# Optimization experiments

Hardware: AMD Instinct MI355X
Metric: run time of the kernel (lower is better)

The kernel has to match this reference:

```python
import jax, jax.numpy as jnp
import numpy as np

T, N, E, IN, ED, H, B, HEADS, L, DFF, OUT = 16, 6400, 65536, 128, 16, 256, 64, 8, 2, 2048, 8
DH = H // HEADS


def _layernorm(x, g, b, eps=1e-5):
    m = jnp.mean(x, -1, keepdims=True)
    v = jnp.var(x, -1, keepdims=True)
    return (x - m) * jax.lax.rsqrt(v + eps) * g + b


def setup_inputs() -> dict:
    key = jax.random.key(0)
    ks = iter(jax.random.split(key, 48))

    def w(shape):
        fan_in = shape[-2] if len(shape) >= 2 else shape[-1]
        return jax.random.normal(next(ks), shape, jnp.float32) * (fan_in ** -0.5)

    inp = {
        "x": jax.random.normal(next(ks), (T, N, IN), jnp.float32),
        "edge_attr": jax.random.normal(next(ks), (T, E, ED), jnp.float32),
        "edge_index": jax.random.randint(next(ks), (T, 2, E), 0, N),
        "batch": jnp.sort(jax.random.randint(next(ks), (T, N), 0, B), axis=-1),
        # EdgeSAGEConv layer 0: msg_in = IN + ED
        "neigh_w0": w((IN + ED, H)), "neigh_b0": jnp.zeros((H,)),
        "root_w0": w((IN, H)), "root_b0": jnp.zeros((H,)),
        "ln_g0": jnp.ones((H,)), "ln_b0": jnp.zeros((H,)),
        # EdgeSAGEConv layer 1: msg_in = H + ED
        "neigh_w1": w((H + ED, H)), "neigh_b1": jnp.zeros((H,)),
        "root_w1": w((H, H)), "root_b1": jnp.zeros((H,)),
        "ln_g1": jnp.ones((H,)), "ln_b1": jnp.zeros((H,)),
        # NodeAttentionPool
        "pool_proj_w": w((H, H)), "pool_proj_b": jnp.zeros((H,)),
        "pool_score_w": w((H, 1)), "pool_score_b": jnp.zeros((1,)),
        # temporal transformer
        "pos_emb": jax.random.normal(next(ks), (T + 1, H), jnp.float32) * 0.02,
        "cls_token": jax.random.normal(next(ks), (1, 1, H), jnp.float32) * 0.02,
        "tx_qkv_w": w((L, H, 3 * H)), "tx_qkv_b": jnp.zeros((L, 3 * H)),
        "tx_out_w": w((L, H, H)), "tx_out_b": jnp.zeros((L, H)),
        "tx_ff1_w": w((L, H, DFF)), "tx_ff1_b": jnp.zeros((L, DFF)),
        "tx_ff2_w": w((L, DFF, H)), "tx_ff2_b": jnp.zeros((L, H)),
        "tx_ln1_g": jnp.ones((L, H)), "tx_ln1_b": jnp.zeros((L, H)),
        "tx_ln2_g": jnp.ones((L, H)), "tx_ln2_b": jnp.zeros((L, H)),
        "head_w": w((H, OUT)), "head_b": jnp.zeros((OUT,)),
    }
    return inp


def reference(x, edge_attr, edge_index, batch,
              neigh_w0, neigh_b0, root_w0, root_b0, ln_g0, ln_b0,
              neigh_w1, neigh_b1, root_w1, root_b1, ln_g1, ln_b1,
              pool_proj_w, pool_proj_b, pool_score_w, pool_score_b,
              pos_emb, cls_token,
              tx_qkv_w, tx_qkv_b, tx_out_w, tx_out_b,
              tx_ff1_w, tx_ff1_b, tx_ff2_w, tx_ff2_b,
              tx_ln1_g, tx_ln1_b, tx_ln2_g, tx_ln2_b,
              head_w, head_b):
    def conv(h, src, dst, ea, wn, bn, wr, br):
        # message: gather x_j, concat edge_attr, linear; aggregate mean at dst
        msg = jnp.concatenate([h[src], ea], -1) @ wn + bn            # [E, H]
        agg = jax.ops.segment_sum(msg, dst, num_segments=N)
        cnt = jax.ops.segment_sum(jnp.ones((dst.shape[0], 1), h.dtype), dst, num_segments=N)
        return agg / jnp.maximum(cnt, 1.0) + h @ wr + br

    def day(xd, eid, ead, bd):
        src, dst = eid[0], eid[1]
        h = _layernorm(jax.nn.relu(conv(xd, src, dst, ead, neigh_w0, neigh_b0, root_w0, root_b0)), ln_g0, ln_b0)
        h = _layernorm(jax.nn.relu(conv(h, src, dst, ead, neigh_w1, neigh_b1, root_w1, root_b1)), ln_g1, ln_b1)
        # segment softmax attention pooling over graphs
        s = (jnp.tanh(h @ pool_proj_w + pool_proj_b) @ pool_score_w + pool_score_b)[:, 0]
        smax = jax.ops.segment_max(s, bd, num_segments=B)
        e = jnp.exp(s - smax[bd])
        wgt = e / jax.ops.segment_sum(e, bd, num_segments=B)[bd]
        return jax.ops.segment_sum(h * wgt[:, None], bd, num_segments=B)  # [B, H]

    Hd = jax.vmap(day)(x, edge_index, edge_attr, batch)               # [T, B, H]
    seq = jnp.transpose(Hd, (1, 0, 2))                                # [B, T, H]
    cls = jnp.broadcast_to(cls_token, (seq.shape[0], 1, H))
    seq = jnp.concatenate([cls, seq], 1) + pos_emb[None]              # [B, T+1, H]
    Bb, S = seq.shape[0], seq.shape[1]
    for l in range(L):  # post-norm TransformerEncoderLayer, relu FFN
        qkv = seq @ tx_qkv_w[l] + tx_qkv_b[l]
        q, k, v = [t.reshape(Bb, S, HEADS, DH) for t in jnp.split(qkv, 3, -1)]
        att = jax.nn.softmax(jnp.einsum('bqhd,bkhd->bhqk', q, k) / (DH ** 0.5), axis=-1)
        o = jnp.einsum('bhqk,bkhd->bqhd', att, v).reshape(Bb, S, H) @ tx_out_w[l] + tx_out_b[l]
        seq = _layernorm(seq + o, tx_ln1_g[l], tx_ln1_b[l])
        f = jax.nn.relu(seq @ tx_ff1_w[l] + tx_ff1_b[l]) @ tx_ff2_w[l] + tx_ff2_b[l]
        seq = _layernorm(seq + f, tx_ln2_g[l], tx_ln2_b[l])
    return jax.nn.softplus(seq[:, 0] @ head_w + head_b)               # [B, OUT]
```

## Files before the change

### kernel.cpp

```cpp
#include <hip/hip_runtime.h>
#include <math.h>

#define T_ 16
#define N_ 6400
#define E_ 65536
#define IN_ 128
#define ED_ 16
#define H_ 256
#define B_ 64
#define HEADS_ 8
#define L_ 2
#define DFF_ 2048
#define OUT_ 8
#define DH_ 32
#define S_ 17
#define M_TX (B_ * S_)

typedef unsigned short u16;
typedef short bf16x8 __attribute__((ext_vector_type(8)));
typedef float f32x4 __attribute__((ext_vector_type(4)));

__device__ __forceinline__ u16 f2bf(float x) {
  unsigned u = __float_as_uint(x);
  unsigned r = (u + 0x7FFFu + ((u >> 16) & 1)) >> 16;
  return (u16)r;
}
__device__ __forceinline__ float bf2f(u16 h) {
  return __uint_as_float(((unsigned)h) << 16);
}

__global__ void zero_k(float* __restrict__ p, long n) {
  long i = (long)blockIdx.x * 256 + threadIdx.x;
  if (i < n) p[i] = 0.f;
}

__global__ void split_k(const float* __restrict__ in, u16* __restrict__ h,
                        u16* __restrict__ l, long n) {
  long i = (long)blockIdx.x * 256 + threadIdx.x;
  if (i < n) {
    const float v = in[i];
    const u16 hi = f2bf(v);
    h[i] = hi;
    l[i] = f2bf(v - bf2f(hi));
  }
}

__launch_bounds__(256) __global__
void wconv_k(const float* __restrict__ W, int K, int Nc, u16* __restrict__ Th,
             u16* __restrict__ Tl, int row_off, int ldk) {
  __shared__ float s[16][17];
  const int kt = blockIdx.y * 16, nt = blockIdx.x * 16;
  const int a = threadIdx.x >> 4, b2 = threadIdx.x & 15;
  s[a][b2] = W[(long)(kt + a) * Nc + nt + b2];
  __syncthreads();
  const float v = s[b2][a];
  const u16 hi = f2bf(v);
  const long o = (long)(row_off + nt + a) * ldk + kt + b2;
  Th[o] = hi;
  Tl[o] = f2bf(v - bf2f(hi));
}

__global__ void biascat_k(const float* __restrict__ b1, const float* __restrict__ b2,
                          float* __restrict__ o) {
  const int i = threadIdx.x;
  o[i] = (i < 256) ? b1[i] : b2[i - 256];
}

template <int EP, int SPLITK, int OUTBF>
__launch_bounds__(256) __global__
void gemm_bf(const u16* __restrict__ Ahb, const u16* __restrict__ Alb, long az,
             const u16* __restrict__ Wth, const u16* __restrict__ Wtl,
             const float* __restrict__ bias,
             float* __restrict__ Ob, u16* __restrict__ Ohb, u16* __restrict__ Olb,
             long oz, int K, int Nc, int ldo) {
  const u16 *Ah, *Al;
  float* O = nullptr;
  u16 *Oh = nullptr, *Ol = nullptr;
  int kbeg, kend;
  if (SPLITK == 1) {
    Ah = Ahb + (long)blockIdx.z * az;
    Al = Alb + (long)blockIdx.z * az;
    if (Ob) O = Ob + (long)blockIdx.z * oz;
    if (Ohb) {
      Oh = Ohb + (long)blockIdx.z * oz;
      Ol = Olb + (long)blockIdx.z * oz;
    }
    kbeg = 0;
    kend = K;
  } else {
    Ah = Ahb;
    Al = Alb;
    O = Ob;
    const int ch = K / SPLITK;
    kbeg = blockIdx.z * ch;
    kend = kbeg + ch;
  }
  const int n0 = blockIdx.x * 128;
  const int m0 = blockIdx.y * 64;
  const int tid = threadIdx.x;
  const int lane = tid & 63;
  const int wave = tid >> 6;
  const int wm = wave & 1;
  const int wn = wave >> 1;
  const int r15 = lane & 15;
  const int q8 = (lane >> 4) << 3;
  const int quad4 = (lane >> 4) << 2;

  __shared__ u16 As_h[64 * 40], As_l[64 * 40];
  __shared__ u16 Bs_h[128 * 40], Bs_l[128 * 40];

  f32x4 acc[2][4];
#pragma unroll
  for (int i = 0; i < 2; ++i)
#pragma unroll
    for (int j = 0; j < 4; ++j) acc[i][j] = (f32x4){0.f, 0.f, 0.f, 0.f};

  const int a_row = tid >> 2;
  const int a_kq = (tid & 3) << 3;
  const int b_row = tid >> 1;
  const int b_kq = (tid & 1) << 4;

  for (int k0 = kbeg; k0 < kend; k0 += 32) {
    const bf16x8 avh = *(const bf16x8*)(Ah + (long)(m0 + a_row) * K + k0 + a_kq);
    const bf16x8 avl = *(const bf16x8*)(Al + (long)(m0 + a_row) * K + k0 + a_kq);
    const long wb = (long)(n0 + b_row) * K + k0 + b_kq;
    const bf16x8 bvh0 = *(const bf16x8*)(Wth + wb);
    const bf16x8 bvh1 = *(const bf16x8*)(Wth + wb + 8);
    const bf16x8 bvl0 = *(const bf16x8*)(Wtl + wb);
    const bf16x8 bvl1 = *(const bf16x8*)(Wtl + wb + 8);
    __syncthreads();
    *(bf16x8*)&As_h[a_row * 40 + a_kq] = avh;
    *(bf16x8*)&As_l[a_row * 40 + a_kq] = avl;
    *(bf16x8*)&Bs_h[b_row * 40 + b_kq] = bvh0;
    *(bf16x8*)&Bs_h[b_row * 40 + b_kq + 8] = bvh1;
    *(bf16x8*)&Bs_l[b_row * 40 + b_kq] = bvl0;
    *(bf16x8*)&Bs_l[b_row * 40 + b_kq + 8] = bvl1;
    __syncthreads();
    bf16x8 ah[2], al[2], bh[4], bl[4];
#pragma unroll
    for (int i = 0; i < 2; ++i) {
      const int ao = (wm * 32 + i * 16 + r15) * 40 + q8;
      ah[i] = *(const bf16x8*)&As_h[ao];
      al[i] = *(const bf16x8*)&As_l[ao];
    }
#pragma unroll
    for (int j = 0; j < 4; ++j) {
      const int bo = (wn * 64 + j * 16 + r15) * 40 + q8;
      bh[j] = *(const bf16x8*)&Bs_h[bo];
      bl[j] = *(const bf16x8*)&Bs_l[bo];
    }
#pragma unroll
    for (int i = 0; i < 2; ++i)
#pragma unroll
      for (int j = 0; j < 4; ++j) {
        acc[i][j] = __builtin_amdgcn_mfma_f32_16x16x32_bf16(ah[i], bh[j], acc[i][j], 0, 0, 0);
        acc[i][j] = __builtin_amdgcn_mfma_f32_16x16x32_bf16(ah[i], bl[j], acc[i][j], 0, 0, 0);
        acc[i][j] = __builtin_amdgcn_mfma_f32_16x16x32_bf16(al[i], bh[j], acc[i][j], 0, 0, 0);
      }
  }

#pragma unroll
  for (int i = 0; i < 2; ++i) {
#pragma unroll
    for (int j = 0; j < 4; ++j) {
      const int col = n0 + wn * 64 + j * 16 + r15;
      const int rbase = m0 + wm * 32 + i * 16 + quad4;
      const float bv = bias ? bias[col] : 0.f;
#pragma unroll
      for (int r = 0; r < 4; ++r) {
        float v = acc[i][j][r];
        if (SPLITK == 1) {
          v += bv;
          if (EP == 1) v = fmaxf(v, 0.f);
          if (EP == 2) v = tanhf(v);
          if (OUTBF) {
            const u16 hi = f2bf(v);
            Oh[(long)(rbase + r) * ldo + col] = hi;
            Ol[(long)(rbase + r) * ldo + col] = f2bf(v - bf2f(hi));
          } else {
            O[(long)(rbase + r) * ldo + col] = v;
          }
        } else {
          if (blockIdx.z == 0) v += bv;
          atomicAdd(&O[(long)(rbase + r) * ldo + col], v);
        }
      }
    }
  }
}

__launch_bounds__(256) __global__
void gemm_k(const float* __restrict__ Abase, long az,
            const float* __restrict__ W,
            const float* __restrict__ addbase, long adz,
            float* __restrict__ Obase, long oz, int K, int Nc, int ldo) {
  const float* A = Abase + (long)blockIdx.z * az;
  const float* addp = addbase + (long)blockIdx.z * adz;
  float* O = Obase + (long)blockIdx.z * oz;
  const int n0 = blockIdx.x * 64;
  const int m0 = blockIdx.y * 64;
  const int tid = threadIdx.x;
  const int tx = tid & 15, ty = tid >> 4;
  __shared__ float As[16][64];
  __shared__ float Ws[16][64];
  float acc[4][4] = {{0.f, 0.f, 0.f, 0.f}, {0.f, 0.f, 0.f, 0.f},
                     {0.f, 0.f, 0.f, 0.f}, {0.f, 0.f, 0.f, 0.f}};
  const int ar = tid >> 2;
  const int ak = (tid & 3) << 2;
  const int wr = tid >> 4;
  const int wc = (tid & 15) << 2;
  for (int k0 = 0; k0 < K; k0 += 16) {
    const float4 av = *(const float4*)(A + (long)(m0 + ar) * K + k0 + ak);
    const float4 wv = *(const float4*)(W + (long)(k0 + wr) * Nc + n0 + wc);
    __syncthreads();
    As[ak + 0][ar] = av.x;
    As[ak + 1][ar] = av.y;
    As[ak + 2][ar] = av.z;
    As[ak + 3][ar] = av.w;
    *(float4*)(&Ws[wr][wc]) = wv;
    __syncthreads();
#pragma unroll
    for (int kk = 0; kk < 16; ++kk) {
      const float4 a4 = *(const float4*)(&As[kk][ty << 2]);
      const float4 b4 = *(const float4*)(&Ws[kk][tx << 2]);
      const float aa[4] = {a4.x, a4.y, a4.z, a4.w};
      const float bb[4] = {b4.x, b4.y, b4.z, b4.w};
#pragma unroll
      for (int i = 0; i < 4; ++i)
#pragma unroll
        for (int j = 0; j < 4; ++j) acc[i][j] = fmaf(aa[i], bb[j], acc[i][j]);
    }
  }
#pragma unroll
  for (int i = 0; i < 4; ++i) {
    const int m = m0 + (ty << 2) + i;
    float o[4];
#pragma unroll
    for (int j = 0; j < 4; ++j)
      o[j] = acc[i][j] + addp[(long)m * ldo + n0 + (tx << 2) + j];
    *(float4*)(O + (long)m * ldo + n0 + (tx << 2)) = make_float4(o[0], o[1], o[2], o[3]);
  }
}

__global__ void deg_k(const int* __restrict__ eib, int* __restrict__ deg, int t0) {
  const int z = blockIdx.y;
  const int e = blockIdx.x * 256 + threadIdx.x;
  const int dst = eib[(long)(t0 + z) * 2 * E_ + E_ + e];
  atomicAdd(&deg[z * N_ + dst], 1);
}

__launch_bounds__(256) __global__
void scan_k(const int* __restrict__ deg, int* __restrict__ offs, int* __restrict__ cursor) {
  const int z = blockIdx.x, tid = threadIdx.x;
  const int* d = deg + (long)z * N_;
  const int base = tid * 25;
  int loc[25];
  int s = 0;
#pragma unroll
  for (int i = 0; i < 25; ++i) {
    loc[i] = s;
    s += d[base + i];
  }
  __shared__ int ps[256];
  ps[tid] = s;
  __syncthreads();
  for (int off = 1; off < 256; off <<= 1) {
    int v = 0;
    if (tid >= off) v = ps[tid - off];
    __syncthreads();
    if (tid >= off) ps[tid] += v;
    __syncthreads();
  }
  const int pre = (tid == 0) ? 0 : ps[tid - 1];
#pragma unroll
  for (int i = 0; i < 25; ++i) {
    const int o = pre + loc[i];
    offs[(long)z * (N_ + 1) + base + i] = o;
    cursor[(long)z * N_ + base + i] = o;
  }
  if (tid == 255) offs[(long)z * (N_ + 1) + N_] = ps[255];
}

__global__ void fill_k(const int* __restrict__ eib, int* __restrict__ cursor,
                       int* __restrict__ elist, int* __restrict__ srcs, int t0) {
  const int z = blockIdx.y;
  const int e = blockIdx.x * 256 + threadIdx.x;
  const int* base = eib + (long)(t0 + z) * 2 * E_;
  const int src = base[e];
  const int dst = base[E_ + e];
  const int slot = atomicAdd(&cursor[z * N_ + dst], 1);
  elist[(long)z * E_ + slot] = e;
  srcs[(long)z * E_ + slot] = src;
}

__global__ void bounds_k(const int* __restrict__ batchb, int* __restrict__ gb, int t0) {
  const int z = blockIdx.x;
  const int g = threadIdx.x;
  if (g > B_) return;
  const int* bt = batchb + (long)(t0 + z) * N_;
  int lo = 0, hi = N_;
  while (lo < hi) {
    const int mid = (lo + hi) >> 1;
    if (bt[mid] < g) lo = mid + 1; else hi = mid;
  }
  gb[z * (B_ + 1) + g] = lo;
}

__launch_bounds__(256) __global__
void eagg_k(const float* __restrict__ eab, const int* __restrict__ elist,
            const int* __restrict__ offs, float* __restrict__ eaggc, int t0) {
  const int z = blockIdx.y;
  const int ln = threadIdx.x >> 4;
  const int c = threadIdx.x & 15;
  const int n = blockIdx.x * 16 + ln;
  const int beg = offs[(long)z * (N_ + 1) + n];
  const int end = offs[(long)z * (N_ + 1) + n + 1];
  const float* ea = eab + (long)(t0 + z) * E_ * ED_;
  const int* el = elist + (long)z * E_;
  float v = 0.f;
  for (int j = beg; j < end; ++j) v += ea[(long)el[j] * ED_ + c];
  eaggc[((long)z * N_ + n) * ED_ + c] = v / fmaxf((float)(end - beg), 1.f);
}

__launch_bounds__(256) __global__
void conv_gather_k(const float* __restrict__ F, const int* __restrict__ srcs,
                   const int* __restrict__ offs, const float* __restrict__ g,
                   const float* __restrict__ bb, u16* __restrict__ outh,
                   u16* __restrict__ outl) {
  const int z = blockIdx.y;
  const int wid = threadIdx.x >> 6;
  const int lane = threadIdx.x & 63;
  const int n = blockIdx.x * 4 + wid;
  const int beg = offs[(long)z * (N_ + 1) + n];
  const int end = offs[(long)z * (N_ + 1) + n + 1];
  const int* sp = srcs + (long)z * E_;
  const float* Fz = F + (long)z * N_ * 512;
  const int co = lane << 2;
  float4 v = make_float4(0.f, 0.f, 0.f, 0.f);
  int j = beg;
  for (; j + 1 < end; j += 2) {
    const int s0 = sp[j], s1 = sp[j + 1];
    const float4 a = *(const float4*)(Fz + (long)s0 * 512 + co);
    const float4 b2 = *(const float4*)(Fz + (long)s1 * 512 + co);
    v.x += a.x + b2.x;
    v.y += a.y + b2.y;
    v.z += a.z + b2.z;
    v.w += a.w + b2.w;
  }
  if (j < end) {
    const float4 a = *(const float4*)(Fz + (long)sp[j] * 512 + co);
    v.x += a.x;
    v.y += a.y;
    v.z += a.z;
    v.w += a.w;
  }
  const float inv = 1.f / fmaxf((float)(end - beg), 1.f);
  const float4 p = *(const float4*)(Fz + (long)n * 512 + 256 + co);
  const float o0 = fmaxf(fmaf(v.x, inv, p.x), 0.f);
  const float o1 = fmaxf(fmaf(v.y, inv, p.y), 0.f);
  const float o2 = fmaxf(fmaf(v.z, inv, p.z), 0.f);
  const float o3 = fmaxf(fmaf(v.w, inv, p.w), 0.f);
  float s = o0 + o1 + o2 + o3;
  float q = o0 * o0 + o1 * o1 + o2 * o2 + o3 * o3;
#pragma unroll
  for (int m = 1; m < 64; m <<= 1) {
    s += __shfl_xor(s, m, 64);
    q += __shfl_xor(q, m, 64);
  }
  const float mean = s * (1.f / H_);
  const float var = q * (1.f / H_) - mean * mean;
  const float r = rsqrtf(var + 1e-5f);
  const float4 gg = *(const float4*)(g + co);
  const float4 bv = *(const float4*)(bb + co);
  float o[4];
  o[0] = (o0 - mean) * r * gg.x + bv.x;
  o[1] = (o1 - mean) * r * gg.y + bv.y;
  o[2] = (o2 - mean) * r * gg.z + bv.z;
  o[3] = (o3 - mean) * r * gg.w + bv.w;
  const long row = ((long)z * N_ + n) * H_ + co;
  ushort4 hv, lv;
  hv.x = f2bf(o[0]); lv.x = f2bf(o[0] - bf2f(hv.x));
  hv.y = f2bf(o[1]); lv.y = f2bf(o[1] - bf2f(hv.y));
  hv.z = f2bf(o[2]); lv.z = f2bf(o[2] - bf2f(hv.z));
  hv.w = f2bf(o[3]); lv.w = f2bf(o[3] - bf2f(hv.w));
  *(ushort4*)(outh + row) = hv;
  *(ushort4*)(outl + row) = lv;
}

__launch_bounds__(256) __global__
void score_k(const float* __restrict__ tnh, const float* __restrict__ sw,
             const float* __restrict__ sb, float* __restrict__ sbuf) {
  const long z = blockIdx.y;
  const int n = blockIdx.x, c = threadIdx.x;
  float p = tnh[(z * N_ + n) * (long)H_ + c] * sw[c];
  __shared__ float rs[256];
  rs[c] = p;
  __syncthreads();
  for (int s = 128; s > 0; s >>= 1) {
    if (c < s) rs[c] += rs[c + s];
    __syncthreads();
  }
  if (c == 0) sbuf[z * N_ + n] = rs[0] + sb[0];
}

__launch_bounds__(256) __global__
void pool_k(const u16* __restrict__ hh, const u16* __restrict__ hl,
            const float* __restrict__ sbuf, const int* __restrict__ gb,
            float* __restrict__ pooled, int t0) {
  const int z = blockIdx.y;
  const int g = blockIdx.x;
  const int c = threadIdx.x;
  const int beg = gb[z * (B_ + 1) + g];
  const int end = gb[z * (B_ + 1) + g + 1];
  const float* sz = sbuf + (long)z * N_;
  __shared__ float red[256];
  float m = -1e30f;
  for (int i = beg + c; i < end; i += 256) m = fmaxf(m, sz[i]);
  red[c] = m;
  __syncthreads();
  for (int s = 128; s > 0; s >>= 1) {
    if (c < s) red[c] = fmaxf(red[c], red[c + s]);
    __syncthreads();
  }
  m = red[0];
  __syncthreads();
  float sum = 0.f;
  for (int i = beg + c; i < end; i += 256) sum += expf(sz[i] - m);
  red[c] = sum;
  __syncthreads();
  for (int s = 128; s > 0; s >>= 1) {
    if (c < s) red[c] += red[c + s];
    __syncthreads();
  }
  sum = red[0];
  float acc = 0.f;
  for (int i = beg; i < end; ++i) {
    const float w = expf(sz[i] - m);
    const long idx = ((long)z * N_ + i) * H_ + c;
    acc = fmaf(bf2f(hh[idx]) + bf2f(hl[idx]), w, acc);
  }
  pooled[((long)(t0 + z) * B_ + g) * H_ + c] = (sum > 0.f) ? acc / sum : 0.f;
}

__global__ void build_seq_k(const float* __restrict__ pooled, const float* __restrict__ cls,
                            const float* __restrict__ pos, float* __restrict__ seq,
                            u16* __restrict__ sh, u16* __restrict__ sl) {
  const int s = blockIdx.x, b = blockIdx.y, c = threadIdx.x;
  const float v0 = (s == 0) ? cls[c] : pooled[(((long)(s - 1)) * B_ + b) * H_ + c];
  const float v = v0 + pos[(long)s * H_ + c];
  const long o = ((long)b * S_ + s) * H_ + c;
  seq[o] = v;
  const u16 hi = f2bf(v);
  sh[o] = hi;
  sl[o] = f2bf(v - bf2f(hi));
}

__launch_bounds__(256) __global__
void attn_k(const float* __restrict__ qkv, u16* __restrict__ oh, u16* __restrict__ ol) {
  const int b = blockIdx.x, h = blockIdx.y;
  __shared__ float qs[S_][DH_], ks[S_][DH_], vs[S_][DH_], att[S_][S_];
  const int tid = threadIdx.x;
  for (int i = tid; i < S_ * DH_; i += 256) {
    const int s = i / DH_, d = i % DH_;
    const long base = ((long)b * S_ + s) * (3 * H_) + h * DH_ + d;
    qs[s][d] = qkv[base];
    ks[s][d] = qkv[base + H_];
    vs[s][d] = qkv[base + 2 * H_];
  }
  __syncthreads();
  for (int i = tid; i < S_ * S_; i += 256) {
    const int r = i / S_, c2 = i % S_;
    float acc = 0.f;
#pragma unroll
    for (int d = 0; d < DH_; ++d) acc = fmaf(qs[r][d], ks[c2][d], acc);
    att[r][c2] = acc * 0.17677669529663687f;
  }
  __syncthreads();
  if (tid < S_) {
    float m = -1e30f;
    for (int j = 0; j < S_; ++j) m = fmaxf(m, att[tid][j]);
    float sum = 0.f;
    for (int j = 0; j < S_; ++j) {
      const float e = expf(att[tid][j] - m);
      att[tid][j] = e;
      sum += e;
    }
    const float inv = 1.f / sum;
    for (int j = 0; j < S_; ++j) att[tid][j] *= inv;
  }
  __syncthreads();
  for (int i = tid; i < S_ * DH_; i += 256) {
    const int s = i / DH_, d = i % DH_;
    float acc = 0.f;
#pragma unroll
    for (int j = 0; j < S_; ++j) acc = fmaf(att[s][j], vs[j][d], acc);
    const long o = ((long)b * S_ + s) * H_ + h * DH_ + d;
    const u16 hi = f2bf(acc);
    oh[o] = hi;
    ol[o] = f2bf(acc - bf2f(hi));
  }
}

__launch_bounds__(256) __global__
void resid_ln_k(float* __restrict__ seq, const float* __restrict__ add,
                const float* __restrict__ g, const float* __restrict__ bb,
                u16* __restrict__ sh, u16* __restrict__ sl) {
  const int row = blockIdx.x, c = threadIdx.x;
  const float v = seq[(long)row * H_ + c] + add[(long)row * H_ + c];
  __shared__ float rs[256], rq[256];
  rs[c] = v;
  rq[c] = v * v;
  __syncthreads();
  for (int s = 128; s > 0; s >>= 1) {
    if (c < s) {
      rs[c] += rs[c + s];
      rq[c] += rq[c + s];
    }
    __syncthreads();
  }
  const float mean = rs[0] * (1.f / H_);
  const float var = rq[0] * (1.f / H_) - mean * mean;
  const float o = (v - mean) * rsqrtf(var + 1e-5f) * g[c] + bb[c];
  const long idx = (long)row * H_ + c;
  seq[idx] = o;
  const u16 hi = f2bf(o);
  sh[idx] = hi;
  sl[idx] = f2bf(o - bf2f(hi));
}

__launch_bounds__(256) __global__
void head_k(const float* __restrict__ seq, const float* __restrict__ hw,
            const float* __restrict__ hb, float* __restrict__ out) {
  const int b = blockIdx.x, c = threadIdx.x;
  const float x = seq[(long)b * S_ * H_ + c];
  __shared__ float rs[256];
  for (int o = 0; o < OUT_; ++o) {
    rs[c] = x * hw[c * OUT_ + o];
    __syncthreads();
    for (int s = 128; s > 0; s >>= 1) {
      if (c < s) rs[c] += rs[c + s];
      __syncthreads();
    }
    if (c == 0) {
      const float v = rs[0] + hb[o];
      out[b * OUT_ + o] = fmaxf(v, 0.f) + log1pf(expf(-fabsf(v)));
    }
    __syncthreads();
  }
}

extern "C" void kernel_launch(void* const* d_in, const int* in_sizes, int n_in,
                              void* d_out, int out_size, void* d_ws, size_t ws_size,
                              hipStream_t stream) {
  const float* x = (const float*)d_in[0];
  const float* ea = (const float*)d_in[1];
  const int* ei = (const int*)d_in[2];
  const int* batch = (const int*)d_in[3];
  const float* nw0 = (const float*)d_in[4];
  const float* nb0 = (const float*)d_in[5];
  const float* rw0 = (const float*)d_in[6];
  const float* rb0 = (const float*)d_in[7];
  const float* lg0 = (const float*)d_in[8];
  const float* lb0 = (const float*)d_in[9];
  const float* nw1 = (const float*)d_in[10];
  const float* nb1 = (const float*)d_in[11];
  const float* rw1 = (const float*)d_in[12];
  const float* rb1 = (const float*)d_in[13];
  const float* lg1 = (const float*)d_in[14];
  const float* lb1 = (const float*)d_in[15];
  const float* ppw = (const float*)d_in[16];
  const float* ppb = (const float*)d_in[17];
  const float* psw = (const float*)d_in[18];
  const float* psb = (const float*)d_in[19];
  const float* pos = (const float*)d_in[20];
  const float* cls = (const float*)d_in[21];
  const float* qkvw = (const float*)d_in[22];
  const float* qkvbias = (const float*)d_in[23];
  const float* outw = (const float*)d_in[24];
  const float* outb = (const float*)d_in[25];
  const float* f1w = (const float*)d_in[26];
  const float* f1b = (const float*)d_in[27];
  const float* f2w = (const float*)d_in[28];
  const float* f2b = (const float*)d_in[29];
  const float* l1g = (const float*)d_in[30];
  const float* l1b = (const float*)d_in[31];
  const float* l2g = (const float*)d_in[32];
  const float* l2b = (const float*)d_in[33];
  const float* hw = (const float*)d_in[34];
  const float* hb = (const float*)d_in[35];
  float* out = (float*)d_out;

  char* cur = (char*)d_ws;
  auto alloc = [&](long bytes) {
    char* p = cur;
    cur += (bytes + 255) & ~255L;
    return (void*)p;
  };
  float* pooled = (float*)alloc((long)T_ * B_ * H_ * 4);
  float* seq = (float*)alloc((long)M_TX * H_ * 4);
  u16* seqh = (u16*)alloc((long)M_TX * H_ * 2);
  u16* seql = (u16*)alloc((long)M_TX * H_ * 2);
  float* qkvbuf = (float*)alloc((long)M_TX * 3 * H_ * 4);
  float* obuf_f = (float*)alloc((long)M_TX * H_ * 4);
  u16* obufh = (u16*)alloc((long)M_TX * H_ * 2);
  u16* obufl = (u16*)alloc((long)M_TX * H_ * 2);
  u16* ffh = (u16*)alloc((long)M_TX * DFF_ * 2);
  u16* ffl = (u16*)alloc((long)M_TX * DFF_ * 2);
  u16* w0ch = (u16*)alloc(512L * 128 * 2);
  u16* w0cl = (u16*)alloc(512L * 128 * 2);
  u16* w1ch = (u16*)alloc(512L * 256 * 2);
  u16* w1cl = (u16*)alloc(512L * 256 * 2);
  u16* ppwh = (u16*)alloc(256L * 256 * 2);
  u16* ppwl = (u16*)alloc(256L * 256 * 2);
  u16* qkvwh = (u16*)alloc((long)L_ * 768 * 256 * 2);
  u16* qkvwl = (u16*)alloc((long)L_ * 768 * 256 * 2);
  u16* outwh = (u16*)alloc((long)L_ * 256 * 256 * 2);
  u16* outwl = (u16*)alloc((long)L_ * 256 * 256 * 2);
  u16* f1wh = (u16*)alloc((long)L_ * 2048 * 256 * 2);
  u16* f1wl = (u16*)alloc((long)L_ * 2048 * 256 * 2);
  u16* f2wh = (u16*)alloc((long)L_ * 256 * 2048 * 2);
  u16* f2wl = (u16*)alloc((long)L_ * 256 * 2048 * 2);
  float* bias0c = (float*)alloc(512 * 4);
  float* bias1c = (float*)alloc(512 * 4);
  const long fixed_used = cur - (char*)d_ws;

  const long perday = (long)N_ * 128 * 2 * 2
                      + (long)N_ * 512 * 4
                      + (long)N_ * 256 * 2 * 2
                      + (long)N_ * 4
                      + (long)N_ * 16 * 4
                      + (2L * E_ + 3L * N_ + (N_ + 1) + (B_ + 1)) * 4 + 4096;
  int DT = 16;
  while (DT > 1 && (size_t)(fixed_used + (long)DT * perday) > ws_size) DT >>= 1;

  u16* xh = (u16*)alloc((long)DT * N_ * 128 * 2);
  u16* xl = (u16*)alloc((long)DT * N_ * 128 * 2);
  float* bufF = (float*)alloc((long)DT * N_ * 512 * 4);
  u16* bufDh = (u16*)alloc((long)DT * N_ * 256 * 2);
  u16* bufDl = (u16*)alloc((long)DT * N_ * 256 * 2);
  float* sbuf = (float*)alloc((long)DT * N_ * 4);
  float* eaggc = (float*)alloc((long)DT * N_ * 16 * 4);
  int* elist = (int*)alloc((long)DT * E_ * 4);
  int* srcs = (int*)alloc((long)DT * E_ * 4);
  int* offs = (int*)alloc((long)DT * (N_ + 1) * 4);
  int* cursor = (int*)alloc((long)DT * N_ * 4);
  int* deg = (int*)alloc((long)DT * N_ * 4);
  int* gb = (int*)alloc((long)DT * (B_ + 1) * 4);

  auto zero = [&](float* p, long n) {
    zero_k<<<dim3((unsigned)((n + 255) / 256)), 256, 0, stream>>>(p, n);
  };

  wconv_k<<<dim3(16, 8), 256, 0, stream>>>(nw0, 128, 256, w0ch, w0cl, 0, 128);
  wconv_k<<<dim3(16, 8), 256, 0, stream>>>(rw0, 128, 256, w0ch, w0cl, 256, 128);
  wconv_k<<<dim3(16, 16), 256, 0, stream>>>(nw1, 256, 256, w1ch, w1cl, 0, 256);
  wconv_k<<<dim3(16, 16), 256, 0, stream>>>(rw1, 256, 256, w1ch, w1cl, 256, 256);
  wconv_k<<<dim3(16, 16), 256, 0, stream>>>(ppw, 256, 256, ppwh, ppwl, 0, 256);
  for (int l = 0; l < L_; ++l) {
    wconv_k<<<dim3(48, 16), 256, 0, stream>>>(qkvw + (long)l * 256 * 768, 256, 768,
                                              qkvwh + (long)l * 768 * 256,
                                              qkvwl + (long)l * 768 * 256, 0, 256);
    wconv_k<<<dim3(16, 16), 256, 0, stream>>>(outw + (long)l * 256 * 256, 256, 256,
                                              outwh + (long)l * 256 * 256,
                                              outwl + (long)l * 256 * 256, 0, 256);
    wconv_k<<<dim3(128, 16), 256, 0, stream>>>(f1w + (long)l * 256 * 2048, 256, 2048,
                                               f1wh + (long)l * 2048 * 256,
                                               f1wl + (long)l * 2048 * 256, 0, 256);
    wconv_k<<<dim3(16, 128), 256, 0, stream>>>(f2w + (long)l * 2048 * 256, 2048, 256,
                                               f2wh + (long)l * 256 * 2048,
                                               f2wl + (long)l * 256 * 2048, 0, 2048);
  }
  biascat_k<<<1, 512, 0, stream>>>(nb0, rb0, bias0c);
  biascat_k<<<1, 512, 0, stream>>>(nb1, rb1, bias1c);

  for (int t0 = 0; t0 < T_; t0 += DT) {
    const int zc = DT;
    zero((float*)deg, (long)zc * N_);
    deg_k<<<dim3(E_ / 256, zc), 256, 0, stream>>>(ei, deg, t0);
    scan_k<<<dim3(zc), 256, 0, stream>>>(deg, offs, cursor);
    fill_k<<<dim3(E_ / 256, zc), 256, 0, stream>>>(ei, cursor, elist, srcs, t0);
    bounds_k<<<dim3(zc), 128, 0, stream>>>(batch, gb, t0);
    eagg_k<<<dim3(N_ / 16, zc), 256, 0, stream>>>(ea, elist, offs, eaggc, t0);
    {
      const long nx = (long)zc * N_ * 128;
      split_k<<<dim3((unsigned)(nx / 256)), 256, 0, stream>>>(
          x + (long)t0 * N_ * IN_, xh, xl, nx);
    }
    gemm_bf<0, 1, 0><<<dim3(4, N_ / 64, zc), 256, 0, stream>>>(
        xh, xl, (long)N_ * 128, w0ch, w0cl, bias0c, bufF, nullptr, nullptr,
        (long)N_ * 512, 128, 512, 512);
    gemm_k<<<dim3(4, N_ / 64, zc), 256, 0, stream>>>(
        eaggc, (long)N_ * 16, nw0 + (long)IN_ * H_, bufF + 256, (long)N_ * 512,
        bufF + 256, (long)N_ * 512, 16, 256, 512);
    conv_gather_k<<<dim3(N_ / 4, zc), 256, 0, stream>>>(bufF, srcs, offs, lg0, lb0,
                                                        bufDh, bufDl);
    gemm_bf<0, 1, 0><<<dim3(4, N_ / 64, zc), 256, 0, stream>>>(
        bufDh, bufDl, (long)N_ * 256, w1ch, w1cl, bias1c, bufF, nullptr, nullptr,
        (long)N_ * 512, 256, 512, 512);
    gemm_k<<<dim3(4, N_ / 64, zc), 256, 0, stream>>>(
        eaggc, (long)N_ * 16, nw1 + (long)H_ * H_, bufF + 256, (long)N_ * 512,
        bufF + 256, (long)N_ * 512, 16, 256, 512);
    conv_gather_k<<<dim3(N_ / 4, zc), 256, 0, stream>>>(bufF, srcs, offs, lg1, lb1,
                                                        bufDh, bufDl);
    gemm_bf<2, 1, 0><<<dim3(2, N_ / 64, zc), 256, 0, stream>>>(
        bufDh, bufDl, (long)N_ * 256, ppwh, ppwl, ppb, bufF, nullptr, nullptr,
        (long)N_ * 256, 256, 256, 256);
    score_k<<<dim3(N_, zc), 256, 0, stream>>>(bufF, psw, psb, sbuf);
    pool_k<<<dim3(B_, zc), 256, 0, stream>>>(bufDh, bufDl, sbuf, gb, pooled, t0);
  }

  build_seq_k<<<dim3(S_, B_), 256, 0, stream>>>(pooled, cls, pos, seq, seqh, seql);
  for (int l = 0; l < L_; ++l) {
    gemm_bf<0, 1, 0><<<dim3(6, M_TX / 64, 1), 256, 0, stream>>>(
        seqh, seql, 0, qkvwh + (long)l * 768 * 256, qkvwl + (long)l * 768 * 256,
        qkvbias + (long)l * 768, qkvbuf, nullptr, nullptr, 0, 256, 768, 768);
    attn_k<<<dim3(B_, HEADS_), 256, 0, stream>>>(qkvbuf, obufh, obufl);
    gemm_bf<0, 1, 0><<<dim3(2, M_TX / 64, 1), 256, 0, stream>>>(
        obufh, obufl, 0, outwh + (long)l * 256 * 256, outwl + (long)l * 256 * 256,
        outb + (long)l * H_, obuf_f, nullptr, nullptr, 0, 256, 256, 256);
    resid_ln_k<<<dim3(M_TX), 256, 0, stream>>>(seq, obuf_f, l1g + (long)l * H_,
                                               l1b + (long)l * H_, seqh, seql);
    gemm_bf<1, 1, 1><<<dim3(16, M_TX / 64, 1), 256, 0, stream>>>(
        seqh, seql, 0, f1wh + (long)l * 2048 * 256, f1wl + (long)l * 2048 * 256,
        f1b + (long)l * DFF_, nullptr, ffh, ffl, 0, 256, 2048, 2048);
    zero(obuf_f, (long)M_TX * H_);
    gemm_bf<0, 8, 0><<<dim3(2, M_TX / 64, 8), 256, 0, stream>>>(
        ffh, ffl, 0, f2wh + (long)l * 256 * 2048, f2wl + (long)l * 256 * 2048,
        f2b + (long)l * H_, obuf_f, nullptr, nullptr, 0, 2048, 256, 256);
    resid_ln_k<<<dim3(M_TX), 256, 0, stream>>>(seq, obuf_f, l2g + (long)l * H_,
                                               l2b + (long)l * H_, seqh, seql);
  }
  head_k<<<dim3(B_), 256, 0, stream>>>(seq, hw, hb, out);
}
```

Baseline: 1.355 ms.

## Fold edge aggregates into GEMM K-dim, fuse pool score, drop LDS staging

Edge-attribute means are written as extra K columns (padded to 160/288) of the bf16 activation buffers, and the weights gain matching rows. This removes the separate fp32 gemm_k passes that added the edge contribution. The attention-pool score (tanh, dot with the score weight, sum) moves into the projection GEMM epilogue via shuffles and atomics, so the tanh buffer write and score_k go away. The GEMM now loads operands straight from global memory with no shared-memory tiles or barriers. That trades LDS reuse for more global and L2 traffic, and the atomic score adds ordering nondeterminism and drops the score bias, which softmax cancels anyway.

```diff
diff --git a/kernel.cpp b/kernel.cpp
--- a/kernel.cpp
+++ b/kernel.cpp
@@ -33,21 +33,27 @@
   long i = (long)blockIdx.x * 256 + threadIdx.x;
   if (i < n) p[i] = 0.f;
 }
-
-__global__ void split_k(const float* __restrict__ in, u16* __restrict__ h,
-                        u16* __restrict__ l, long n) {
+__global__ void wzero_k(u16* __restrict__ p, long n) {
+  long i = (long)blockIdx.x * 256 + threadIdx.x;
+  if (i < n) p[i] = 0;
+}
+
+__global__ void splitx_k(const float* __restrict__ in, u16* __restrict__ h,
+                         u16* __restrict__ l, long n) {
   long i = (long)blockIdx.x * 256 + threadIdx.x;
   if (i < n) {
+    const long row = i >> 7;
+    const int c = (int)(i & 127);
     const float v = in[i];
     const u16 hi = f2bf(v);
-    h[i] = hi;
-    l[i] = f2bf(v - bf2f(hi));
-  }
-}
-
-__launch_bounds__(256) __global__
-void wconv_k(const float* __restrict__ W, int K, int Nc, u16* __restrict__ Th,
-             u16* __restrict__ Tl, int row_off, int ldk) {
+    h[row * 160 + c] = hi;
+    l[row * 160 + c] = f2bf(v - bf2f(hi));
+  }
+}
+
+__launch_bounds__(256) __global__
+void wtrans_k(const float* __restrict__ W, int Nc, u16* __restrict__ Th,
+              u16* __restrict__ Tl, int row_off, int k_off, int ldk) {
   __shared__ float s[16][17];
   const int kt = blockIdx.y * 16, nt = blockIdx.x * 16;
   const int a = threadIdx.x >> 4, b2 = threadIdx.x & 15;
@@ -55,7 +61,7 @@
   __syncthreads();
   const float v = s[b2][a];
   const u16 hi = f2bf(v);
-  const long o = (long)(row_off + nt + a) * ldk + kt + b2;
+  const long o = (long)(row_off + nt + a) * ldk + k_off + kt + b2;
   Th[o] = hi;
   Tl[o] = f2bf(v - bf2f(hi));
 }
@@ -68,33 +74,11 @@
 
 template <int EP, int SPLITK, int OUTBF>
 __launch_bounds__(256) __global__
-void gemm_bf(const u16* __restrict__ Ahb, const u16* __restrict__ Alb, long az,
-             const u16* __restrict__ Wth, const u16* __restrict__ Wtl,
-             const float* __restrict__ bias,
-             float* __restrict__ Ob, u16* __restrict__ Ohb, u16* __restrict__ Olb,
-             long oz, int K, int Nc, int ldo) {
-  const u16 *Ah, *Al;
-  float* O = nullptr;
-  u16 *Oh = nullptr, *Ol = nullptr;
-  int kbeg, kend;
-  if (SPLITK == 1) {
-    Ah = Ahb + (long)blockIdx.z * az;
-    Al = Alb + (long)blockIdx.z * az;
-    if (Ob) O = Ob + (long)blockIdx.z * oz;
-    if (Ohb) {
-      Oh = Ohb + (long)blockIdx.z * oz;
-      Ol = Olb + (long)blockIdx.z * oz;
-    }
-    kbeg = 0;
-    kend = K;
-  } else {
-    Ah = Ahb;
-    Al = Alb;
-    O = Ob;
-    const int ch = K / SPLITK;
-    kbeg = blockIdx.z * ch;
-    kend = kbeg + ch;
-  }
+void gemm_flat(const u16* __restrict__ Ah, const u16* __restrict__ Al, int lda,
+               const u16* __restrict__ Wth, const u16* __restrict__ Wtl, int ldw,
+               const float* __restrict__ bias,
+               float* __restrict__ O, u16* __restrict__ Oh, u16* __restrict__ Ol,
+               int ldo, int K, float* __restrict__ sc, const float* __restrict__ scw) {
   const int n0 = blockIdx.x * 128;
   const int m0 = blockIdx.y * 64;
   const int tid = threadIdx.x;
@@ -106,8 +90,29 @@
   const int q8 = (lane >> 4) << 3;
   const int quad4 = (lane >> 4) << 2;
 
-  __shared__ u16 As_h[64 * 40], As_l[64 * 40];
-  __shared__ u16 Bs_h[128 * 40], Bs_l[128 * 40];
+  int kbeg = 0, kend = K;
+  if (SPLITK > 1) {
+    const int ch = K / SPLITK;
+    kbeg = blockIdx.z * ch;
+    kend = kbeg + ch;
+  }
+
+  const u16* arh[2];
+  const u16* arl[2];
+  const u16* brh[4];
+  const u16* brl[4];
+#pragma unroll
+  for (int i = 0; i < 2; ++i) {
+    const long o = (long)(m0 + wm * 32 + i * 16 + r15) * lda + q8;
+    arh[i] = Ah + o;
+    arl[i] = Al + o;
+  }
+#pragma unroll
+  for (int j = 0; j < 4; ++j) {
+    const long o = (long)(n0 + wn * 64 + j * 16 + r15) * ldw + q8;
+    brh[j] = Wth + o;
+    brl[j] = Wtl + o;
+  }
 
   f32x4 acc[2][4];
 #pragma unroll
@@ -115,39 +120,17 @@
 #pragma unroll
     for (int j = 0; j < 4; ++j) acc[i][j] = (f32x4){0.f, 0.f, 0.f, 0.f};
 
-  const int a_row = tid >> 2;
-  const int a_kq = (tid & 3) << 3;
-  const int b_row = tid >> 1;
-  const int b_kq = (tid & 1) << 4;
-
   for (int k0 = kbeg; k0 < kend; k0 += 32) {
-    const bf16x8 avh = *(const bf16x8*)(Ah + (long)(m0 + a_row) * K + k0 + a_kq);
-    const bf16x8 avl = *(const bf16x8*)(Al + (long)(m0 + a_row) * K + k0 + a_kq);
-    const long wb = (long)(n0 + b_row) * K + k0 + b_kq;
-    const bf16x8 bvh0 = *(const bf16x8*)(Wth + wb);
-    const bf16x8 bvh1 = *(const bf16x8*)(Wth + wb + 8);
-    const bf16x8 bvl0 = *(const bf16x8*)(Wtl + wb);
-    const bf16x8 bvl1 = *(const bf16x8*)(Wtl + wb + 8);
-    __syncthreads();
-    *(bf16x8*)&As_h[a_row * 40 + a_kq] = avh;
-    *(bf16x8*)&As_l[a_row * 40 + a_kq] = avl;
-    *(bf16x8*)&Bs_h[b_row * 40 + b_kq] = bvh0;
-    *(bf16x8*)&Bs_h[b_row * 40 + b_kq + 8] = bvh1;
-    *(bf16x8*)&Bs_l[b_row * 40 + b_kq] = bvl0;
-    *(bf16x8*)&Bs_l[b_row * 40 + b_kq + 8] = bvl1;
-    __syncthreads();
     bf16x8 ah[2], al[2], bh[4], bl[4];
 #pragma unroll
     for (int i = 0; i < 2; ++i) {
-      const int ao = (wm * 32 + i * 16 + r15) * 40 + q8;
-      ah[i] = *(const bf16x8*)&As_h[ao];
-      al[i] = *(const bf16x8*)&As_l[ao];
+      ah[i] = *(const bf16x8*)(arh[i] + k0);
+      al[i] = *(const bf16x8*)(arl[i] + k0);
     }
 #pragma unroll
     for (int j = 0; j < 4; ++j) {
-      const int bo = (wn * 64 + j * 16 + r15) * 40 + q8;
-      bh[j] = *(const bf16x8*)&Bs_h[bo];
-      bl[j] = *(const bf16x8*)&Bs_l[bo];
+      bh[j] = *(const bf16x8*)(brh[j] + k0);
+      bl[j] = *(const bf16x8*)(brl[j] + k0);
     }
 #pragma unroll
     for (int i = 0; i < 2; ++i)
@@ -159,6 +142,26 @@
       }
   }
 
+  if (EP == 3) {
+#pragma unroll
+    for (int i = 0; i < 2; ++i) {
+#pragma unroll
+      for (int r = 0; r < 4; ++r) {
+        float part = 0.f;
+#pragma unroll
+        for (int j = 0; j < 4; ++j) {
+          const int col = n0 + wn * 64 + j * 16 + r15;
+          part += tanhf(acc[i][j][r] + bias[col]) * scw[col];
+        }
+#pragma unroll
+        for (int m = 1; m < 16; m <<= 1) part += __shfl_xor(part, m, 64);
+        if (r15 == 0)
+          atomicAdd(&sc[m0 + wm * 32 + i * 16 + quad4 + r], part);
+      }
+    }
+    return;
+  }
+
 #pragma unroll
   for (int i = 0; i < 2; ++i) {
 #pragma unroll
@@ -172,7 +175,6 @@
         if (SPLITK == 1) {
           v += bv;
           if (EP == 1) v = fmaxf(v, 0.f);
-          if (EP == 2) v = tanhf(v);
           if (OUTBF) {
             const u16 hi = f2bf(v);
             Oh[(long)(rbase + r) * ldo + col] = hi;
@@ -189,59 +191,6 @@
   }
 }
 
-__launch_bounds__(256) __global__
-void gemm_k(const float* __restrict__ Abase, long az,
-            const float* __restrict__ W,
-            const float* __restrict__ addbase, long adz,
-            float* __restrict__ Obase, long oz, int K, int Nc, int ldo) {
-  const float* A = Abase + (long)blockIdx.z * az;
-  const float* addp = addbase + (long)blockIdx.z * adz;
-  float* O = Obase + (long)blockIdx.z * oz;
-  const int n0 = blockIdx.x * 64;
-  const int m0 = blockIdx.y * 64;
-  const int tid = threadIdx.x;
-  const int tx = tid & 15, ty = tid >> 4;
-  __shared__ float As[16][64];
-  __shared__ float Ws[16][64];
-  float acc[4][4] = {{0.f, 0.f, 0.f, 0.f}, {0.f, 0.f, 0.f, 0.f},
-                     {0.f, 0.f, 0.f, 0.f}, {0.f, 0.f, 0.f, 0.f}};
-  const int ar = tid >> 2;
-  const int ak = (tid & 3) << 2;
-  const int wr = tid >> 4;
-  const int wc = (tid & 15) << 2;
-  for (int k0 = 0; k0 < K; k0 += 16) {
-    const float4 av = *(const float4*)(A + (long)(m0 + ar) * K + k0 + ak);
-    const float4 wv = *(const float4*)(W + (long)(k0 + wr) * Nc + n0 + wc);
-    __syncthreads();
-    As[ak + 0][ar] = av.x;
-    As[ak + 1][ar] = av.y;
-    As[ak + 2][ar] = av.z;
-    As[ak + 3][ar] = av.w;
-    *(float4*)(&Ws[wr][wc]) = wv;
-    __syncthreads();
-#pragma unroll
-    for (int kk = 0; kk < 16; ++kk) {
-      const float4 a4 = *(const float4*)(&As[kk][ty << 2]);
-      const float4 b4 = *(const float4*)(&Ws[kk][tx << 2]);
-      const float aa[4] = {a4.x, a4.y, a4.z, a4.w};
-      const float bb[4] = {b4.x, b4.y, b4.z, b4.w};
-#pragma unroll
-      for (int i = 0; i < 4; ++i)
-#pragma unroll
-        for (int j = 0; j < 4; ++j) acc[i][j] = fmaf(aa[i], bb[j], acc[i][j]);
-    }
-  }
-#pragma unroll
-  for (int i = 0; i < 4; ++i) {
-    const int m = m0 + (ty << 2) + i;
-    float o[4];
-#pragma unroll
-    for (int j = 0; j < 4; ++j)
-      o[j] = acc[i][j] + addp[(long)m * ldo + n0 + (tx << 2) + j];
-    *(float4*)(O + (long)m * ldo + n0 + (tx << 2)) = make_float4(o[0], o[1], o[2], o[3]);
-  }
-}
-
 __global__ void deg_k(const int* __restrict__ eib, int* __restrict__ deg, int t0) {
   const int z = blockIdx.y;
   const int e = blockIdx.x * 256 + threadIdx.x;
@@ -308,18 +257,29 @@
 
 __launch_bounds__(256) __global__
 void eagg_k(const float* __restrict__ eab, const int* __restrict__ elist,
-            const int* __restrict__ offs, float* __restrict__ eaggc, int t0) {
+            const int* __restrict__ offs,
+            u16* __restrict__ h0, u16* __restrict__ l0,
+            u16* __restrict__ h1, u16* __restrict__ l1, int t0) {
   const int z = blockIdx.y;
-  const int ln = threadIdx.x >> 4;
-  const int c = threadIdx.x & 15;
-  const int n = blockIdx.x * 16 + ln;
-  const int beg = offs[(long)z * (N_ + 1) + n];
-  const int end = offs[(long)z * (N_ + 1) + n + 1];
-  const float* ea = eab + (long)(t0 + z) * E_ * ED_;
-  const int* el = elist + (long)z * E_;
+  const int ln = threadIdx.x >> 5;
+  const int c = threadIdx.x & 31;
+  const int n = blockIdx.x * 8 + ln;
   float v = 0.f;
-  for (int j = beg; j < end; ++j) v += ea[(long)el[j] * ED_ + c];
-  eaggc[((long)z * N_ + n) * ED_ + c] = v / fmaxf((float)(end - beg), 1.f);
+  if (c < ED_) {
+    const int beg = offs[(long)z * (N_ + 1) + n];
+    const int end = offs[(long)z * (N_ + 1) + n + 1];
+    const float* ea = eab + (long)(t0 + z) * E_ * ED_;
+    const int* el = elist + (long)z * E_;
+    for (int j = beg; j < end; ++j) v += ea[(long)el[j] * ED_ + c];
+    v /= fmaxf((float)(end - beg), 1.f);
+  }
+  const u16 hi = f2bf(v);
+  const u16 lo = f2bf(v - bf2f(hi));
+  const long row = (long)z * N_ + n;
+  h0[row * 160 + 128 + c] = hi;
+  l0[row * 160 + 128 + c] = lo;
+  h1[row * 288 + 256 + c] = hi;
+  l1[row * 288 + 256 + c] = lo;
 }
 
 __launch_bounds__(256) __global__
@@ -377,7 +337,7 @@
   o[1] = (o1 - mean) * r * gg.y + bv.y;
   o[2] = (o2 - mean) * r * gg.z + bv.z;
   o[3] = (o3 - mean) * r * gg.w + bv.w;
-  const long row = ((long)z * N_ + n) * H_ + co;
+  const long row = ((long)z * N_ + n) * 288 + co;
   ushort4 hv, lv;
   hv.x = f2bf(o[0]); lv.x = f2bf(o[0] - bf2f(hv.x));
   hv.y = f2bf(o[1]); lv.y = f2bf(o[1] - bf2f(hv.y));
@@ -385,22 +345,6 @@
   hv.w = f2bf(o[3]); lv.w = f2bf(o[3] - bf2f(hv.w));
   *(ushort4*)(outh + row) = hv;
   *(ushort4*)(outl + row) = lv;
-}
-
-__launch_bounds__(256) __global__
-void score_k(const float* __restrict__ tnh, const float* __restrict__ sw,
-             const float* __restrict__ sb, float* __restrict__ sbuf) {
-  const long z = blockIdx.y;
-  const int n = blockIdx.x, c = threadIdx.x;
-  float p = tnh[(z * N_ + n) * (long)H_ + c] * sw[c];
-  __shared__ float rs[256];
-  rs[c] = p;
-  __syncthreads();
-  for (int s = 128; s > 0; s >>= 1) {
-    if (c < s) rs[c] += rs[c + s];
-    __syncthreads();
-  }
-  if (c == 0) sbuf[z * N_ + n] = rs[0] + sb[0];
 }
 
 __launch_bounds__(256) __global__
@@ -436,7 +380,7 @@
   float acc = 0.f;
   for (int i = beg; i < end; ++i) {
     const float w = expf(sz[i] - m);
-    const long idx = ((long)z * N_ + i) * H_ + c;
+    const long idx = ((long)z * N_ + i) * 288 + c;
     acc = fmaf(bf2f(hh[idx]) + bf2f(hl[idx]), w, acc);
   }
   pooled[((long)(t0 + z) * B_ + g) * H_ + c] = (sum > 0.f) ? acc / sum : 0.f;
@@ -571,7 +515,6 @@
   const float* ppw = (const float*)d_in[16];
   const float* ppb = (const float*)d_in[17];
   const float* psw = (const float*)d_in[18];
-  const float* psb = (const float*)d_in[19];
   const float* pos = (const float*)d_in[20];
   const float* cls = (const float*)d_in[21];
   const float* qkvw = (const float*)d_in[22];
@@ -606,10 +549,10 @@
   u16* obufl = (u16*)alloc((long)M_TX * H_ * 2);
   u16* ffh = (u16*)alloc((long)M_TX * DFF_ * 2);
   u16* ffl = (u16*)alloc((long)M_TX * DFF_ * 2);
-  u16* w0ch = (u16*)alloc(512L * 128 * 2);
-  u16* w0cl = (u16*)alloc(512L * 128 * 2);
-  u16* w1ch = (u16*)alloc(512L * 256 * 2);
-  u16* w1cl = (u16*)alloc(512L * 256 * 2);
+  u16* w0h = (u16*)alloc(512L * 160 * 2);
+  u16* w0l = (u16*)alloc(512L * 160 * 2);
+  u16* w1h = (u16*)alloc(512L * 288 * 2);
+  u16* w1l = (u16*)alloc(512L * 288 * 2);
   u16* ppwh = (u16*)alloc(256L * 256 * 2);
   u16* ppwl = (u16*)alloc(256L * 256 * 2);
   u16* qkvwh = (u16*)alloc((long)L_ * 768 * 256 * 2);
@@ -624,22 +567,20 @@
   float* bias1c = (float*)alloc(512 * 4);
   const long fixed_used = cur - (char*)d_ws;
 
-  const long perday = (long)N_ * 128 * 2 * 2
+  const long perday = (long)N_ * 160 * 2 * 2
                       + (long)N_ * 512 * 4
-                      + (long)N_ * 256 * 2 * 2
+                      + (long)N_ * 288 * 2 * 2
                       + (long)N_ * 4
-                      + (long)N_ * 16 * 4
-                      + (2L * E_ + 3L * N_ + (N_ + 1) + (B_ + 1)) * 4 + 4096;
+                      + (2L * E_ + 3L * N_ + (N_ + 1) + (B_ + 1)) * 4 + 8192;
   int DT = 16;
   while (DT > 1 && (size_t)(fixed_used + (long)DT * perday) > ws_size) DT >>= 1;
 
-  u16* xh = (u16*)alloc((long)DT * N_ * 128 * 2);
-  u16* xl = (u16*)alloc((long)DT * N_ * 128 * 2);
+  u16* xh = (u16*)alloc((long)DT * N_ * 160 * 2);
+  u16* xl = (u16*)alloc((long)DT * N_ * 160 * 2);
   float* bufF = (float*)alloc((long)DT * N_ * 512 * 4);
-  u16* bufDh = (u16*)alloc((long)DT * N_ * 256 * 2);
-  u16* bufDl = (u16*)alloc((long)DT * N_ * 256 * 2);
+  u16* bufDh = (u16*)alloc((long)DT * N_ * 288 * 2);
+  u16* bufDl = (u16*)alloc((long)DT * N_ * 288 * 2);
   float* sbuf = (float*)alloc((long)DT * N_ * 4);
-  float* eaggc = (float*)alloc((long)DT * N_ * 16 * 4);
   int* elist = (int*)alloc((long)DT * E_ * 4);
   int* srcs = (int*)alloc((long)DT * E_ * 4);
   int* offs = (int*)alloc((long)DT * (N_ + 1) * 4);
@@ -651,24 +592,30 @@
     zero_k<<<dim3((unsigned)((n + 255) / 256)), 256, 0, stream>>>(p, n);
   };
 
-  wconv_k<<<dim3(16, 8), 256, 0, stream>>>(nw0, 128, 256, w0ch, w0cl, 0, 128);
-  wconv_k<<<dim3(16, 8), 256, 0, stream>>>(rw0, 128, 256, w0ch, w0cl, 256, 128);
-  wconv_k<<<dim3(16, 16), 256, 0, stream>>>(nw1, 256, 256, w1ch, w1cl, 0, 256);
-  wconv_k<<<dim3(16, 16), 256, 0, stream>>>(rw1, 256, 256, w1ch, w1cl, 256, 256);
-  wconv_k<<<dim3(16, 16), 256, 0, stream>>>(ppw, 256, 256, ppwh, ppwl, 0, 256);
+  wzero_k<<<dim3((unsigned)((512L * 160 + 255) / 256)), 256, 0, stream>>>(w0h, 512L * 160);
+  wzero_k<<<dim3((unsigned)((512L * 160 + 255) / 256)), 256, 0, stream>>>(w0l, 512L * 160);
+  wzero_k<<<dim3((unsigned)((512L * 288 + 255) / 256)), 256, 0, stream>>>(w1h, 512L * 288);
+  wzero_k<<<dim3((unsigned)((512L * 288 + 255) / 256)), 256, 0, stream>>>(w1l, 512L * 288);
+  wtrans_k<<<dim3(16, 8), 256, 0, stream>>>(nw0, 256, w0h, w0l, 0, 0, 160);
+  wtrans_k<<<dim3(16, 8), 256, 0, stream>>>(rw0, 256, w0h, w0l, 256, 0, 160);
+  wtrans_k<<<dim3(16, 1), 256, 0, stream>>>(nw0 + 128L * 256, 256, w0h, w0l, 256, 128, 160);
+  wtrans_k<<<dim3(16, 16), 256, 0, stream>>>(nw1, 256, w1h, w1l, 0, 0, 288);
+  wtrans_k<<<dim3(16, 16), 256, 0, stream>>>(rw1, 256, w1h, w1l, 256, 0, 288);
+  wtrans_k<<<dim3(16, 1), 256, 0, stream>>>(nw1 + 256L * 256, 256, w1h, w1l, 256, 256, 288);
+  wtrans_k<<<dim3(16, 16), 256, 0, stream>>>(ppw, 256, ppwh, ppwl, 0, 0, 256);
   for (int l = 0; l < L_; ++l) {
-    wconv_k<<<dim3(48, 16), 256, 0, stream>>>(qkvw + (long)l * 256 * 768, 256, 768,
-                                              qkvwh + (long)l * 768 * 256,
-                                              qkvwl + (long)l * 768 * 256, 0, 256);
-    wconv_k<<<dim3(16, 16), 256, 0, stream>>>(outw + (long)l * 256 * 256, 256, 256,
-                                              outwh + (long)l * 256 * 256,
-                                              outwl + (long)l * 256 * 256, 0, 256);
-    wconv_k<<<dim3(128, 16), 256, 0, stream>>>(f1w + (long)l * 256 * 2048, 256, 2048,
-                                               f1wh + (long)l * 2048 * 256,
-                                               f1wl + (long)l * 2048 * 256, 0, 256);
-    wconv_k<<<dim3(16, 128), 256, 0, stream>>>(f2w + (long)l * 2048 * 256, 2048, 256,
-                                               f2wh + (long)l * 256 * 2048,
-                                               f2wl + (long)l * 256 * 2048, 0, 2048);
+    wtrans_k<<<dim3(48, 16), 256, 0, stream>>>(qkvw + (long)l * 256 * 768, 768,
+                                               qkvwh + (long)l * 768 * 256,
+                                               qkvwl + (long)l * 768 * 256, 0, 0, 256);
+    wtrans_k<<<dim3(16, 16), 256, 0, stream>>>(outw + (long)l * 256 * 256, 256,
+                                               outwh + (long)l * 256 * 256,
+                                               outwl + (long)l * 256 * 256, 0, 0, 256);
+    wtrans_k<<<dim3(128, 16), 256, 0, stream>>>(f1w + (long)l * 256 * 2048, 2048,
+                                                f1wh + (long)l * 2048 * 256,
+                                                f1wl + (long)l * 2048 * 256, 0, 0, 256);
+    wtrans_k<<<dim3(16, 128), 256, 0, stream>>>(f2w + (long)l * 2048 * 256, 256,
+                                                f2wh + (long)l * 256 * 2048,
+                                                f2wl + (long)l * 256 * 2048, 0, 0, 2048);
   }
   biascat_k<<<1, 512, 0, stream>>>(nb0, rb0, bias0c);
   biascat_k<<<1, 512, 0, stream>>>(nb1, rb1, bias1c);
@@ -680,53 +627,47 @@
     scan_k<<<dim3(zc), 256, 0, stream>>>(deg, offs, cursor);
     fill_k<<<dim3(E_ / 256, zc), 256, 0, stream>>>(ei, cursor, elist, srcs, t0);
     bounds_k<<<dim3(zc), 128, 0, stream>>>(batch, gb, t0);
-    eagg_k<<<dim3(N_ / 16, zc), 256, 0, stream>>>(ea, elist, offs, eaggc, t0);
     {
       const long nx = (long)zc * N_ * 128;
-      split_k<<<dim3((unsigned)(nx / 256)), 256, 0, stream>>>(
-          x + (long)t0 * N_ * IN_, xh, xl, nx);
-    }
-    gemm_bf<0, 1, 0><<<dim3(4, N_ / 64, zc), 256, 0, stream>>>(
-        xh, xl, (long)N_ * 128, w0ch, w0cl, bias0c, bufF, nullptr, nullptr,
-        (long)N_ * 512, 128, 512, 512);
-    gemm_k<<<dim3(4, N_ / 64, zc), 256, 0, stream>>>(
-        eaggc, (long)N_ * 16, nw0 + (long)IN_ * H_, bufF + 256, (long)N_ * 512,
-        bufF + 256, (long)N_ * 512, 16, 256, 512);
+      splitx_k<<<dim3((unsigned)(nx / 256)), 256, 0, stream>>>(x + (long)t0 * N_ * IN_,
+                                                               xh, xl, nx);
+    }
+    eagg_k<<<dim3(N_ / 8, zc), 256, 0, stream>>>(ea, elist, offs, xh, xl, bufDh, bufDl, t0);
+    gemm_flat<0, 1, 0><<<dim3(4, zc * (N_ / 64)), 256, 0, stream>>>(
+        xh, xl, 160, w0h, w0l, 160, bias0c, bufF, nullptr, nullptr, 512, 160,
+        nullptr, nullptr);
     conv_gather_k<<<dim3(N_ / 4, zc), 256, 0, stream>>>(bufF, srcs, offs, lg0, lb0,
                                                         bufDh, bufDl);
-    gemm_bf<0, 1, 0><<<dim3(4, N_ / 64, zc), 256, 0, stream>>>(
-        bufDh, bufDl, (long)N_ * 256, w1ch, w1cl, bias1c, bufF, nullptr, nullptr,
-        (long)N_ * 512, 256, 512, 512);
-    gemm_k<<<dim3(4, N_ / 64, zc), 256, 0, stream>>>(
-        eaggc, (long)N_ * 16, nw1 + (long)H_ * H_, bufF + 256, (long)N_ * 512,
-        bufF + 256, (long)N_ * 512, 16, 256, 512);
+    gemm_flat<0, 1, 0><<<dim3(4, zc * (N_ / 64)), 256, 0, stream>>>(
+        bufDh, bufDl, 288, w1h, w1l, 288, bias1c, bufF, nullptr, nullptr, 512, 288,
+        nullptr, nullptr);
     conv_gather_k<<<dim3(N_ / 4, zc), 256, 0, stream>>>(bufF, srcs, offs, lg1, lb1,
                                                         bufDh, bufDl);
-    gemm_bf<2, 1, 0><<<dim3(2, N_ / 64, zc), 256, 0, stream>>>(
-        bufDh, bufDl, (long)N_ * 256, ppwh, ppwl, ppb, bufF, nullptr, nullptr,
-        (long)N_ * 256, 256, 256, 256);
-    score_k<<<dim3(N_, zc), 256, 0, stream>>>(bufF, psw, psb, sbuf);
+    zero(sbuf, (long)zc * N_);
+    gemm_flat<3, 1, 0><<<dim3(2, zc * (N_ / 64)), 256, 0, stream>>>(
+        bufDh, bufDl, 288, ppwh, ppwl, 256, ppb, nullptr, nullptr, nullptr, 0, 256,
+        sbuf, psw);
     pool_k<<<dim3(B_, zc), 256, 0, stream>>>(bufDh, bufDl, sbuf, gb, pooled, t0);
   }
 
   build_seq_k<<<dim3(S_, B_), 256, 0, stream>>>(pooled, cls, pos, seq, seqh, seql);
   for (int l = 0; l < L_; ++l) {
-    gemm_bf<0, 1, 0><<<dim3(6, M_TX / 64, 1), 256, 0, stream>>>(
-        seqh, seql, 0, qkvwh + (long)l * 768 * 256, qkvwl + (long)l * 768 * 256,
-        qkvbias + (long)l * 768, qkvbuf, nullptr, nullptr, 0, 256, 768, 768);
+    gemm_flat<0, 1, 0><<<dim3(6, M_TX / 64), 256, 0, stream>>>(
+        seqh, seql, 256, qkvwh + (long)l * 768 * 256, qkvwl + (long)l * 768 * 256, 256,
+        qkvbias + (long)l * 768, qkvbuf, nullptr, nullptr, 768, 256, nullptr, nullptr);
     attn_k<<<dim3(B_, HEADS_), 256, 0, stream>>>(qkvbuf, obufh, obufl);
-    gemm_bf<0, 1, 0><<<dim3(2, M_TX / 64, 1), 256, 0, stream>>>(
-        obufh, obufl, 0, outwh + (long)l * 256 * 256, outwl + (long)l * 256 * 256,
-        outb + (long)l * H_, obuf_f, nullptr, nullptr, 0, 256, 256, 256);
+    gemm_flat<0, 1, 0><<<dim3(2, M_TX / 64), 256, 0, stream>>>(
+        obufh, obufl, 256, outwh + (long)l * 256 * 256, outwl + (long)l * 256 * 256, 256,
+        outb + (long)l * H_, obuf_f, nullptr, nullptr, 256, 256, nullptr, nullptr);
     resid_ln_k<<<dim3(M_TX), 256, 0, stream>>>(seq, obuf_f, l1g + (long)l * H_,
                                                l1b + (long)l * H_, seqh, seql);
-    gemm_bf<1, 1, 1><<<dim3(16, M_TX / 64, 1), 256, 0, stream>>>(
-        seqh, seql, 0, f1wh + (long)l * 2048 * 256, f1wl + (long)l * 2048 * 256,
-        f1b + (long)l * DFF_, nullptr, ffh, ffl, 0, 256, 2048, 2048);
+    gemm_flat<1, 1, 1><<<dim3(16, M_TX / 64), 256, 0, stream>>>(
+        seqh, seql, 256, f1wh + (long)l * 2048 * 256, f1wl + (long)l * 2048 * 256, 256,
+        f1b + (long)l * DFF_, nullptr, ffh, ffl, 2048, 256, nullptr, nullptr);
     zero(obuf_f, (long)M_TX * H_);
-    gemm_bf<0, 8, 0><<<dim3(2, M_TX / 64, 8), 256, 0, stream>>>(
-        ffh, ffl, 0, f2wh + (long)l * 256 * 2048, f2wl + (long)l * 256 * 2048,
-        f2b + (long)l * H_, obuf_f, nullptr, nullptr, 0, 2048, 256, 256);
+    gemm_flat<0, 8, 0><<<dim3(2, M_TX / 64, 8), 256, 0, stream>>>(
+        ffh, ffl, 2048, f2wh + (long)l * 256 * 2048, f2wl + (long)l * 256 * 2048, 2048,
+        f2b + (long)l * H_, obuf_f, nullptr, nullptr, 256, 2048, nullptr, nullptr);
     resid_ln_k<<<dim3(M_TX), 256, 0, stream>>>(seq, obuf_f, l2g + (long)l * H_,
                                                l2b + (long)l * H_, seqh, seql);
   }
```

Measured after the change: 1.595 ms. 17.7% more time.
